# Kernel tuning notes

Hardware: AMD Instinct MI355X
Metric: run time of the kernel (lower is better)

Reference implementation:

```python
import jax, jax.numpy as jnp
import numpy as np


def setup_inputs() -> dict:
    key = jax.random.key(0)
    k1, k2 = jax.random.split(key)
    B, L = 16384, 4096
    logits = jax.random.normal(k1, (B, L), dtype=jnp.float32)
    targets = jax.random.randint(k2, (B, L), 0, 2, dtype=jnp.int32)
    return {"logits": logits, "targets": targets}


def reference(logits, targets):
    # For each positive label p in row i:
    #   loss = -log_softmax([l_ip] ++ neg_logits_i)[0]
    #        = logsumexp(pos, negs) - pos = softplus(neg_lse_i - l_ip)
    pos_mask = targets == 1
    neg_mask = targets == 0
    # per-row logsumexp over negative logits; -inf if row has no negatives
    neg_lse = jax.nn.logsumexp(logits, axis=1, where=neg_mask)  # [B]
    per_pos = jax.nn.softplus(neg_lse[:, None] - logits)        # [B, L]
    total = jnp.sum(jnp.where(pos_mask, per_pos, 0.0))
    num_pos = jnp.sum(pos_mask)
    return jnp.where(num_pos > 0,
                     total / jnp.maximum(num_pos, 1).astype(logits.dtype),
                     jnp.array(0.0, logits.dtype))
```

## Files before the change

kernel.cpp:

```cpp
#include <hip/hip_runtime.h>
#include <math.h>

#define ROWS 16384
#define COLS 4096
#define BLOCK 256
#define EPT 16

__global__ __launch_bounds__(BLOCK) void row_loss_kernel(
        const float* __restrict__ logits,
        const int* __restrict__ targets,
        double* __restrict__ part_sum,
        int* __restrict__ part_cnt) {
    const int tid = threadIdx.x;
    const int row = blockIdx.x;
    const size_t base = (size_t)row * COLS;

    const float4* lg4 = reinterpret_cast<const float4*>(logits + base);
    const int4*   tg4 = reinterpret_cast<const int4*>(targets + base);

    float v[EPT];
    unsigned posmask = 0u;
    unsigned negmask = 0u;
    #pragma unroll
    for (int p = 0; p < 4; ++p) {
        float4 l = lg4[tid + p * BLOCK];
        int4   t = tg4[tid + p * BLOCK];
        v[p * 4 + 0] = l.x; v[p * 4 + 1] = l.y;
        v[p * 4 + 2] = l.z; v[p * 4 + 3] = l.w;
        posmask |= (t.x == 1 ? 1u : 0u) << (p * 4 + 0);
        posmask |= (t.y == 1 ? 1u : 0u) << (p * 4 + 1);
        posmask |= (t.z == 1 ? 1u : 0u) << (p * 4 + 2);
        posmask |= (t.w == 1 ? 1u : 0u) << (p * 4 + 3);
        negmask |= (t.x == 0 ? 1u : 0u) << (p * 4 + 0);
        negmask |= (t.y == 0 ? 1u : 0u) << (p * 4 + 1);
        negmask |= (t.z == 0 ? 1u : 0u) << (p * 4 + 2);
        negmask |= (t.w == 0 ? 1u : 0u) << (p * 4 + 3);
    }

    __shared__ float  sredf[4];
    __shared__ double sredd[4];
    __shared__ int    sredi[4];
    const int wave = tid >> 6;
    const int lane = tid & 63;

    float m = -INFINITY;
    #pragma unroll
    for (int j = 0; j < EPT; ++j)
        if ((negmask >> j) & 1u) m = fmaxf(m, v[j]);
    #pragma unroll
    for (int off = 32; off; off >>= 1)
        m = fmaxf(m, __shfl_xor(m, off));
    if (lane == 0) sredf[wave] = m;
    __syncthreads();
    m = fmaxf(fmaxf(sredf[0], sredf[1]), fmaxf(sredf[2], sredf[3]));

    float s = 0.0f;
    #pragma unroll
    for (int j = 0; j < EPT; ++j) {
        float e = __expf(v[j] - m);
        s += ((negmask >> j) & 1u) ? e : 0.0f;
    }
    #pragma unroll
    for (int off = 32; off; off >>= 1)
        s += __shfl_xor(s, off);
    __syncthreads();
    if (lane == 0) sredf[wave] = s;
    __syncthreads();
    s = (sredf[0] + sredf[1]) + (sredf[2] + sredf[3]);

    float neg_lse = m + __logf(s);

    float local = 0.0f;
    int   c = __popc(posmask);
    #pragma unroll
    for (int j = 0; j < EPT; ++j) {
        float x  = neg_lse - v[j];
        float sp = fmaxf(x, 0.0f) + __logf(1.0f + __expf(-fabsf(x)));
        local += ((posmask >> j) & 1u) ? sp : 0.0f;
    }
    #pragma unroll
    for (int off = 32; off; off >>= 1) {
        local += __shfl_xor(local, off);
        c     += __shfl_xor(c, off);
    }
    if (lane == 0) { sredd[wave] = (double)local; sredi[wave] = c; }
    __syncthreads();

    if (tid == 0) {
        part_sum[row] = (sredd[0] + sredd[1]) + (sredd[2] + sredd[3]);
        part_cnt[row] = (sredi[0] + sredi[1]) + (sredi[2] + sredi[3]);
    }
}

__global__ __launch_bounds__(1024) void reduce_kernel(
        const double* __restrict__ part_sum,
        const int* __restrict__ part_cnt,
        float* __restrict__ out) {
    const int tid  = threadIdx.x;
    const int wave = tid >> 6;
    const int lane = tid & 63;

    double s = 0.0;
    long long c = 0;
    for (int i = tid; i < ROWS; i += 1024) {
        s += part_sum[i];
        c += part_cnt[i];
    }
    #pragma unroll
    for (int off = 32; off; off >>= 1) {
        s += __shfl_xor(s, off);
        c += __shfl_xor(c, off);
    }
    __shared__ double sd[16];
    __shared__ long long sc[16];
    if (lane == 0) { sd[wave] = s; sc[wave] = c; }
    __syncthreads();
    if (tid == 0) {
        double ts = 0.0;
        long long tc = 0;
        #pragma unroll
        for (int w = 0; w < 16; ++w) { ts += sd[w]; tc += sc[w]; }
        out[0] = (tc > 0) ? (float)(ts / (double)tc) : 0.0f;
    }
}

extern "C" void kernel_launch(void* const* d_in, const int* in_sizes, int n_in,
                              void* d_out, int out_size, void* d_ws, size_t ws_size,
                              hipStream_t stream) {
    const float* logits  = (const float*)d_in[0];
    const int*   targets = (const int*)d_in[1];
    float* out = (float*)d_out;

    double* part_sum = (double*)d_ws;
    int*    part_cnt = (int*)((char*)d_ws + ROWS * sizeof(double));

    row_loss_kernel<<<ROWS, BLOCK, 0, stream>>>(logits, targets, part_sum, part_cnt);
    reduce_kernel<<<1, 1024, 0, stream>>>(part_sum, part_cnt, out);
}
```

Before: 104.8 us.

## Process one row per wavefront to eliminate block-level shared-memory reductions

New measurement: 120.3 us. +14.7%, slower.

```diff
diff --git a/kernel.cpp b/kernel.cpp
--- a/kernel.cpp
+++ b/kernel.cpp
@@ -3,92 +3,79 @@
 
 #define ROWS 16384
 #define COLS 4096
-#define BLOCK 256
-#define EPT 16
+#define WPB 4
+#define BLOCK (WPB * 64)
+#define F4L 16
 
 __global__ __launch_bounds__(BLOCK) void row_loss_kernel(
         const float* __restrict__ logits,
         const int* __restrict__ targets,
         double* __restrict__ part_sum,
         int* __restrict__ part_cnt) {
-    const int tid = threadIdx.x;
-    const int row = blockIdx.x;
+    const int lane = threadIdx.x & 63;
+    const int wave = threadIdx.x >> 6;
+    const int row  = blockIdx.x * WPB + wave;
     const size_t base = (size_t)row * COLS;
 
     const float4* lg4 = reinterpret_cast<const float4*>(logits + base);
     const int4*   tg4 = reinterpret_cast<const int4*>(targets + base);
 
-    float v[EPT];
-    unsigned posmask = 0u;
-    unsigned negmask = 0u;
+    float v[64];
+    unsigned long long posmask = 0ull;
+    unsigned long long negmask = 0ull;
     #pragma unroll
-    for (int p = 0; p < 4; ++p) {
-        float4 l = lg4[tid + p * BLOCK];
-        int4   t = tg4[tid + p * BLOCK];
-        v[p * 4 + 0] = l.x; v[p * 4 + 1] = l.y;
-        v[p * 4 + 2] = l.z; v[p * 4 + 3] = l.w;
-        posmask |= (t.x == 1 ? 1u : 0u) << (p * 4 + 0);
-        posmask |= (t.y == 1 ? 1u : 0u) << (p * 4 + 1);
-        posmask |= (t.z == 1 ? 1u : 0u) << (p * 4 + 2);
-        posmask |= (t.w == 1 ? 1u : 0u) << (p * 4 + 3);
-        negmask |= (t.x == 0 ? 1u : 0u) << (p * 4 + 0);
-        negmask |= (t.y == 0 ? 1u : 0u) << (p * 4 + 1);
-        negmask |= (t.z == 0 ? 1u : 0u) << (p * 4 + 2);
-        negmask |= (t.w == 0 ? 1u : 0u) << (p * 4 + 3);
+    for (int k = 0; k < F4L; ++k) {
+        float4 l = lg4[lane + 64 * k];
+        int4   t = tg4[lane + 64 * k];
+        v[4 * k + 0] = l.x; v[4 * k + 1] = l.y;
+        v[4 * k + 2] = l.z; v[4 * k + 3] = l.w;
+        unsigned pm = (unsigned)(t.x == 1) | ((unsigned)(t.y == 1) << 1) |
+                      ((unsigned)(t.z == 1) << 2) | ((unsigned)(t.w == 1) << 3);
+        unsigned nm = (unsigned)(t.x == 0) | ((unsigned)(t.y == 0) << 1) |
+                      ((unsigned)(t.z == 0) << 2) | ((unsigned)(t.w == 0) << 3);
+        posmask |= (unsigned long long)pm << (4 * k);
+        negmask |= (unsigned long long)nm << (4 * k);
     }
-
-    __shared__ float  sredf[4];
-    __shared__ double sredd[4];
-    __shared__ int    sredi[4];
-    const int wave = tid >> 6;
-    const int lane = tid & 63;
 
     float m = -INFINITY;
     #pragma unroll
-    for (int j = 0; j < EPT; ++j)
-        if ((negmask >> j) & 1u) m = fmaxf(m, v[j]);
+    for (int j = 0; j < 64; ++j) {
+        float cand = ((negmask >> j) & 1ull) ? v[j] : -INFINITY;
+        m = fmaxf(m, cand);
+    }
     #pragma unroll
     for (int off = 32; off; off >>= 1)
         m = fmaxf(m, __shfl_xor(m, off));
-    if (lane == 0) sredf[wave] = m;
-    __syncthreads();
-    m = fmaxf(fmaxf(sredf[0], sredf[1]), fmaxf(sredf[2], sredf[3]));
 
     float s = 0.0f;
     #pragma unroll
-    for (int j = 0; j < EPT; ++j) {
+    for (int j = 0; j < 64; ++j) {
         float e = __expf(v[j] - m);
-        s += ((negmask >> j) & 1u) ? e : 0.0f;
+        s += ((negmask >> j) & 1ull) ? e : 0.0f;
     }
     #pragma unroll
     for (int off = 32; off; off >>= 1)
         s += __shfl_xor(s, off);
-    __syncthreads();
-    if (lane == 0) sredf[wave] = s;
-    __syncthreads();
-    s = (sredf[0] + sredf[1]) + (sredf[2] + sredf[3]);
 
-    float neg_lse = m + __logf(s);
+    const float neg_lse = m + __logf(s);
 
     float local = 0.0f;
-    int   c = __popc(posmask);
     #pragma unroll
-    for (int j = 0; j < EPT; ++j) {
+    for (int j = 0; j < 64; ++j) {
         float x  = neg_lse - v[j];
         float sp = fmaxf(x, 0.0f) + __logf(1.0f + __expf(-fabsf(x)));
-        local += ((posmask >> j) & 1u) ? sp : 0.0f;
+        local += ((posmask >> j) & 1ull) ? sp : 0.0f;
     }
+    int c = __popcll(posmask);
     #pragma unroll
     for (int off = 32; off; off >>= 1) {
         local += __shfl_xor(local, off);
         c     += __shfl_xor(c, off);
     }
-    if (lane == 0) { sredd[wave] = (double)local; sredi[wave] = c; }
-    __syncthreads();
 
-    if (tid == 0) {
-        part_sum[row] = (sredd[0] + sredd[1]) + (sredd[2] + sredd[3]);
-        part_cnt[row] = (sredi[0] + sredi[1]) + (sredi[2] + sredi[3]);
+    if (lane == 0) {
+        part_sum[row] = (double)local;
+        part_cnt[row] = c;
     }
 }
 
@@ -134,6 +121,6 @@
     double* part_sum = (double*)d_ws;
     int*    part_cnt = (int*)((char*)d_ws + ROWS * sizeof(double));
 
-    row_loss_kernel<<<ROWS, BLOCK, 0, stream>>>(logits, targets, part_sum, part_cnt);
+    row_loss_kernel<<<ROWS / WPB, BLOCK, 0, stream>>>(logits, targets, part_sum, part_cnt);
     reduce_kernel<<<1, 1024, 0, stream>>>(part_sum, part_cnt, out);
 }
```
